# Optimization experiments

Measured on AMD Instinct MI355X. Metric: run time of the kernel, lower is better.

## Reference

```python
import jax, jax.numpy as jnp
import numpy as np

T, H, I, E, K = 1024, 2048, 1024, 16, 2

def setup_inputs() -> dict:
    key = jax.random.key(0)
    ks = jax.random.split(key, 6)
    return {
        "hidden_states": jax.random.normal(ks[0], (T, H), jnp.float32),
        "gate_w": jax.random.normal(ks[1], (E, H), jnp.float32) * 0.02,
        "bias": jax.random.normal(ks[2], (E,), jnp.float32) * 0.01,
        "w1": jax.random.normal(ks[3], (E, H, I), jnp.float32) * 0.02,
        "w3": jax.random.normal(ks[4], (E, H, I), jnp.float32) * 0.02,
        "w2": jax.random.normal(ks[5], (E, I, H), jnp.float32) * 0.02,
    }

def reference(hidden_states, gate_w, bias, w1, w3, w2):
    x = hidden_states  # [T, H]
    # Router gating linear in fp32 (gate.weight cast to float32 in source)
    logits = x.astype(jnp.float32) @ gate_w.T            # [T, E]
    scores = jax.nn.softmax(logits, axis=-1)             # scoring_func='softmax'
    # grouped_topk with num_expert_group=topk_group=1 == plain top-k;
    # e_score_correction_bias only biases expert *selection*.
    _, topk_idx = jax.lax.top_k(scores + bias[None, :], K)   # [T, K]
    topk_w = jnp.take_along_axis(scores, topk_idx, axis=1)   # weights from raw scores
    topk_w = topk_w / jnp.sum(topk_w, axis=-1, keepdims=True)  # renormalize=True
    # Scatter top-k weights into dense combine matrix [T, E]
    rows = jnp.arange(T)[:, None]
    combine = jnp.zeros((T, E), jnp.float32).at[rows, topk_idx].add(topk_w)
    # SwiGLU experts computed densely over all experts, masked by combine
    h1 = jnp.einsum('th,ehi->eti', x, w1)                # [E, T, I]
    h3 = jnp.einsum('th,ehi->eti', x, w3)
    he = jax.nn.silu(h1) * h3
    ye = jnp.einsum('eti,eih->eth', he, w2)              # [E, T, H]
    out = jnp.einsum('eth,te->th', ye, combine.astype(x.dtype))  # weighted combine
    return out
```

## Files before the change

### kernel.cpp

```cpp
#include <hip/hip_runtime.h>
#include <stdint.h>

#define Ttok 1024
#define Hdim 2048
#define Idim 1024
#define Enum 16

typedef __attribute__((ext_vector_type(8))) short  short8;
typedef __attribute__((ext_vector_type(4))) float  f32x4;

#define BAR() asm volatile("s_waitcnt lgkmcnt(0)\n\ts_barrier" ::: "memory")

__device__ __forceinline__ unsigned short f2bf(float f) {
    union { float f; uint32_t u; } v; v.f = f;
    uint32_t u = v.u;
    return (unsigned short)((u + 0x7FFFu + ((u >> 16) & 1u)) >> 16);
}
__device__ __forceinline__ float bf2f(unsigned short h) {
    union { uint32_t u; float f; } v; v.u = ((uint32_t)h) << 16; return v.f;
}
__device__ __forceinline__ uint32_t cvtpk(float lo, float hi) {
    uint32_t d;
    asm("v_cvt_pk_bf16_f32 %0, %1, %2" : "=v"(d) : "v"(lo), "v"(hi));
    return d;
}
__device__ __forceinline__ float silu_mul(unsigned short h1u, unsigned short h3u) {
    float h1 = bf2f(h1u), h3 = bf2f(h3u);
    return h1 * h3 * __builtin_amdgcn_rcpf(1.f + __expf(-h1));
}

__global__ __launch_bounds__(256) void k_router(
    const float* __restrict__ x, const float* __restrict__ gw,
    const float* __restrict__ bias,
    int* __restrict__ counts, int* __restrict__ tids, float* __restrict__ tws)
{
    __shared__ __align__(16) float xrow[Hdim];
    __shared__ float lg[Enum];
    const int t = blockIdx.x;
    const float* xr = x + (size_t)t * Hdim;

    for (int i = threadIdx.x; i < Hdim / 4; i += 256)
        ((f32x4*)xrow)[i] = ((const f32x4*)xr)[i];
    __syncthreads();

    const int lane = threadIdx.x & 63;
    const int wid  = threadIdx.x >> 6;
    for (int e = wid; e < Enum; e += 4) {
        const float* g = gw + (size_t)e * Hdim;
        float s = 0.f;
        for (int j = lane; j < Hdim; j += 64) s += xrow[j] * g[j];
        #pragma unroll
        for (int off = 32; off; off >>= 1) s += __shfl_xor(s, off);
        if (lane == 0) lg[e] = s;
    }
    __syncthreads();

    if (threadIdx.x == 0) {
        float m = lg[0];
        #pragma unroll
        for (int e = 1; e < Enum; ++e) m = fmaxf(m, lg[e]);
        float sc[Enum]; float sum = 0.f;
        #pragma unroll
        for (int e = 0; e < Enum; ++e) { float ex = expf(lg[e] - m); sc[e] = ex; sum += ex; }
        float inv = 1.f / sum;
        #pragma unroll
        for (int e = 0; e < Enum; ++e) sc[e] *= inv;
        int i0 = 0; float b0 = sc[0] + bias[0];
        #pragma unroll
        for (int e = 1; e < Enum; ++e) { float bb = sc[e] + bias[e]; if (bb > b0) { b0 = bb; i0 = e; } }
        int i1 = -1; float b1 = -1e30f;
        #pragma unroll
        for (int e = 0; e < Enum; ++e) {
            if (e == i0) continue;
            float bb = sc[e] + bias[e]; if (bb > b1) { b1 = bb; i1 = e; }
        }
        float w0 = sc[i0], w1v = sc[i1];
        float winv = 1.f / (w0 + w1v);
        w0 *= winv; w1v *= winv;
        int p0 = atomicAdd(&counts[i0], 1);
        tids[i0 * Ttok + p0] = t; tws[i0 * Ttok + p0] = w0;
        int p1 = atomicAdd(&counts[i1], 1);
        tids[i1 * Ttok + p1] = t; tws[i1 * Ttok + p1] = w1v;
    }
}

__global__ __launch_bounds__(256) void k_gather(
    const float* __restrict__ x, const int* __restrict__ counts,
    const int* __restrict__ tids, unsigned short* __restrict__ Xg)
{
    const int p = blockIdx.y;
    int pe = -1, c = 0, acc = 0;
    #pragma unroll
    for (int j = 0; j < Enum; ++j) {
        int nj = (counts[j] + 63) >> 6;
        if (pe < 0 && p < acc + nj) { pe = j; c = p - acc; }
        acc += nj;
    }
    if (pe < 0) return;
    const int Ne = counts[pe];
    const int s  = blockIdx.x;
    const int r  = threadIdx.x & 63;
    const int kq = threadIdx.x >> 6;
    const int row = c * 64 + r;
    const bool valid = row < Ne;
    const int tok = valid ? tids[pe * Ttok + row] : 0;
    const float* xr = x + (size_t)tok * Hdim;

    #pragma unroll
    for (int j = 0; j < 8; ++j) {
        int kg = s * 32 + j * 4 + kq;
        uint4 o = make_uint4(0, 0, 0, 0);
        if (valid) {
            f32x4 p0 = *(const f32x4*)(xr + kg * 8);
            f32x4 p1 = *(const f32x4*)(xr + kg * 8 + 4);
            o.x = cvtpk(p0[0], p0[1]); o.y = cvtpk(p0[2], p0[3]);
            o.z = cvtpk(p1[0], p1[1]); o.w = cvtpk(p1[2], p1[3]);
        }
        *(uint4*)(Xg + ((size_t)(p * 256 + kg) * 64 + r) * 8) = o;
    }
}

union ShH {
    struct {
        unsigned short Xs[2][4096];
        unsigned short Ws[2][8][64][8];
    } a;
    unsigned short T[64][80];
};

__global__ __launch_bounds__(256, 4) void k_h(
    const unsigned short* __restrict__ Xg,
    const float* __restrict__ w1, const float* __restrict__ w3,
    const int* __restrict__ counts,
    unsigned short* __restrict__ H1, unsigned short* __restrict__ H3)
{
    const int e  = blockIdx.z;
    const int Ne = counts[e];
    const int c  = blockIdx.y;
    if (c * 64 >= Ne) return;
    int poff = 0;
    #pragma unroll
    for (int j = 0; j < Enum; ++j) if (j < e) poff += (counts[j] + 63) >> 6;
    const int pc   = poff + c;
    const int mat  = blockIdx.x >> 4;
    const int cb   = blockIdx.x & 15;
    const int col0 = cb * 64;
    const int tid  = threadIdx.x;
    const int lane = tid & 63;
    const int wid  = tid >> 6;
    const int l15  = lane & 15;
    const int kq   = lane >> 4;

    __shared__ ShH sh;

    const unsigned short* xsrc = Xg + (size_t)pc * 131072;
    const int wkg = tid >> 5;
    const int wcp = (tid & 31) * 2;
    const float* wsrc = (mat ? w3 : w1)
        + ((size_t)e * Hdim + wkg * 8) * Idim + col0 + wcp;
    unsigned short* Hm = mat ? H3 : H1;

    f32x4 acc[4];
    #pragma unroll
    for (int a = 0; a < 4; ++a) acc[a] = (f32x4)(0.f);

    const int NK = Hdim / 64;

    auto xload = [&](int ks, short8& v0, short8& v1) {
        const unsigned short* p = xsrc + (size_t)ks * 4096;
        v0 = *(const short8*)(p + tid * 8);
        v1 = *(const short8*)(p + 2048 + tid * 8);
    };
    auto wload = [&](int ks, float2* wv) {
        const float* wp = wsrc + (size_t)ks * 64 * Idim;
        #pragma unroll
        for (int j = 0; j < 8; ++j) wv[j] = *(const float2*)(wp + (size_t)j * Idim);
    };
    auto stage = [&](int buf, short8 x0, short8 x1, const float2* wv) {
        *(short8*)&sh.a.Xs[buf][tid * 8]        = x0;
        *(short8*)&sh.a.Xs[buf][2048 + tid * 8] = x1;
        uint4 q0, q1;
        q0.x = cvtpk(wv[0].x, wv[1].x); q0.y = cvtpk(wv[2].x, wv[3].x);
        q0.z = cvtpk(wv[4].x, wv[5].x); q0.w = cvtpk(wv[6].x, wv[7].x);
        q1.x = cvtpk(wv[0].y, wv[1].y); q1.y = cvtpk(wv[2].y, wv[3].y);
        q1.z = cvtpk(wv[4].y, wv[5].y); q1.w = cvtpk(wv[6].y, wv[7].y);
        *(uint4*)&sh.a.Ws[buf][wkg][wcp][0]     = q0;
        *(uint4*)&sh.a.Ws[buf][wkg][wcp + 1][0] = q1;
    };
    auto mfma_step = [&](int buf) {
        #pragma unroll
        for (int ks2 = 0; ks2 < 2; ++ks2) {
            const int kgi = ks2 * 4 + kq;
            short8 b = *(const short8*)&sh.a.Ws[buf][kgi][wid * 16 + l15][0];
            #pragma unroll
            for (int fr = 0; fr < 4; ++fr) {
                short8 af = *(const short8*)&sh.a.Xs[buf][kgi * 512 + (fr * 16 + l15) * 8];
                acc[fr] = __builtin_amdgcn_mfma_f32_16x16x32_bf16(af, b, acc[fr], 0, 0, 0);
            }
        }
    };

    short8 xA0, xA1, xB0, xB1;
    float2 wA[8], wB[8];
    xload(0, xA0, xA1); wload(0, wA);
    xload(1, xB0, xB1); wload(1, wB);
    stage(0, xA0, xA1, wA);
    BAR();

    for (int ks = 0; ks < NK; ks += 2) {
        if (ks + 2 < NK) { xload(ks + 2, xA0, xA1); wload(ks + 2, wA); }
        mfma_step(0);
        stage(1, xB0, xB1, wB);
        BAR();
        if (ks + 3 < NK) { xload(ks + 3, xB0, xB1); wload(ks + 3, wB); }
        mfma_step(1);
        if (ks + 2 < NK) stage(0, xA0, xA1, wA);
        BAR();
    }

    #pragma unroll
    for (int fr = 0; fr < 4; ++fr)
        #pragma unroll
        for (int k = 0; k < 4; ++k)
            sh.T[fr * 16 + kq * 4 + k][wid * 16 + l15] = f2bf(acc[fr][k]);
    __syncthreads();
    {
        const int r = tid & 63, kgw = tid >> 6;
        #pragma unroll
        for (int q = 0; q < 2; ++q) {
            int KGl = kgw * 2 + q;
            short8 v = *(const short8*)&sh.T[r][KGl * 8];
            *(short8*)(Hm + ((size_t)(pc * 128 + cb * 8 + KGl) * 64 + r) * 8) = v;
        }
    }
}

__global__ __launch_bounds__(256, 4) void k_o(
    const unsigned short* __restrict__ H1, const unsigned short* __restrict__ H3,
    const float* __restrict__ w2,
    const int* __restrict__ counts, const int* __restrict__ tids,
    const float* __restrict__ tws,
    float* __restrict__ out)
{
    const int e  = blockIdx.z;
    const int Ne = counts[e];
    const int c  = blockIdx.y;
    if (c * 64 >= Ne) return;
    int poff = 0;
    #pragma unroll
    for (int j = 0; j < Enum; ++j) if (j < e) poff += (counts[j] + 63) >> 6;
    const int pc   = poff + c;
    const int col0 = blockIdx.x * 64;
    const int tid  = threadIdx.x;
    const int lane = tid & 63;
    const int wid  = tid >> 6;
    const int l15  = lane & 15;
    const int kq   = lane >> 4;

    __shared__ __align__(16) unsigned short As[2][4096];
    __shared__ __align__(16) unsigned short Ws[2][8][64][8];

    const unsigned short* h1src = H1 + (size_t)pc * 65536;
    const unsigned short* h3src = H3 + (size_t)pc * 65536;
    const int wkg = tid >> 5;
    const int wcp = (tid & 31) * 2;
    const float* wsrc = w2 + ((size_t)e * Idim + wkg * 8) * Hdim + col0 + wcp;

    f32x4 acc[4];
    #pragma unroll
    for (int a = 0; a < 4; ++a) acc[a] = (f32x4)(0.f);

    const int NK = Idim / 64;

    auto hload = [&](int ks, short8& a0, short8& a1, short8& b0, short8& b1) {
        a0 = *(const short8*)(h1src + (size_t)ks * 4096 + tid * 8);
        a1 = *(const short8*)(h1src + (size_t)ks * 4096 + 2048 + tid * 8);
        b0 = *(const short8*)(h3src + (size_t)ks * 4096 + tid * 8);
        b1 = *(const short8*)(h3src + (size_t)ks * 4096 + 2048 + tid * 8);
    };
    auto wload = [&](int ks, float2* wv) {
        const float* wp = wsrc + (size_t)ks * 64 * Hdim;
        #pragma unroll
        for (int j = 0; j < 8; ++j) wv[j] = *(const float2*)(wp + (size_t)j * Hdim);
    };
    auto stage = [&](int buf, short8 h10, short8 h11, short8 h30, short8 h31,
                     const float2* wv) {
        uint4 o0, o1;
        o0.x = cvtpk(silu_mul(h10[0], h30[0]), silu_mul(h10[1], h30[1]));
        o0.y = cvtpk(silu_mul(h10[2], h30[2]), silu_mul(h10[3], h30[3]));
        o0.z = cvtpk(silu_mul(h10[4], h30[4]), silu_mul(h10[5], h30[5]));
        o0.w = cvtpk(silu_mul(h10[6], h30[6]), silu_mul(h10[7], h30[7]));
        o1.x = cvtpk(silu_mul(h11[0], h31[0]), silu_mul(h11[1], h31[1]));
        o1.y = cvtpk(silu_mul(h11[2], h31[2]), silu_mul(h11[3], h31[3]));
        o1.z = cvtpk(silu_mul(h11[4], h31[4]), silu_mul(h11[5], h31[5]));
        o1.w = cvtpk(silu_mul(h11[6], h31[6]), silu_mul(h11[7], h31[7]));
        *(uint4*)&As[buf][tid * 8]        = o0;
        *(uint4*)&As[buf][2048 + tid * 8] = o1;
        uint4 q0, q1;
        q0.x = cvtpk(wv[0].x, wv[1].x); q0.y = cvtpk(wv[2].x, wv[3].x);
        q0.z = cvtpk(wv[4].x, wv[5].x); q0.w = cvtpk(wv[6].x, wv[7].x);
        q1.x = cvtpk(wv[0].y, wv[1].y); q1.y = cvtpk(wv[2].y, wv[3].y);
        q1.z = cvtpk(wv[4].y, wv[5].y); q1.w = cvtpk(wv[6].y, wv[7].y);
        *(uint4*)&Ws[buf][wkg][wcp][0]     = q0;
        *(uint4*)&Ws[buf][wkg][wcp + 1][0] = q1;
    };
    auto mfma_step = [&](int buf) {
        #pragma unroll
        for (int ks2 = 0; ks2 < 2; ++ks2) {
            const int kgi = ks2 * 4 + kq;
            short8 b = *(const short8*)&Ws[buf][kgi][wid * 16 + l15][0];
            #pragma unroll
            for (int fr = 0; fr < 4; ++fr) {
                short8 af = *(const short8*)&As[buf][kgi * 512 + (fr * 16 + l15) * 8];
                acc[fr] = __builtin_amdgcn_mfma_f32_16x16x32_bf16(af, b, acc[fr], 0, 0, 0);
            }
        }
    };

    short8 h1A0, h1A1, h3A0, h3A1, h1B0, h1B1, h3B0, h3B1;
    float2 wA[8], wB[8];
    hload(0, h1A0, h1A1, h3A0, h3A1); wload(0, wA);
    hload(1, h1B0, h1B1, h3B0, h3B1); wload(1, wB);
    stage(0, h1A0, h1A1, h3A0, h3A1, wA);
    BAR();

    for (int ks = 0; ks < NK; ks += 2) {
        if (ks + 2 < NK) { hload(ks + 2, h1A0, h1A1, h3A0, h3A1); wload(ks + 2, wA); }
        mfma_step(0);
        stage(1, h1B0, h1B1, h3B0, h3B1, wB);
        BAR();
        if (ks + 3 < NK) { hload(ks + 3, h1B0, h1B1, h3B0, h3B1); wload(ks + 3, wB); }
        mfma_step(1);
        if (ks + 2 < NK) stage(0, h1A0, h1A1, h3A0, h3A1, wA);
        BAR();
    }

    #pragma unroll
    for (int fr = 0; fr < 4; ++fr) {
        #pragma unroll
        for (int k = 0; k < 4; ++k) {
            int grow = c * 64 + fr * 16 + kq * 4 + k;
            if (grow < Ne) {
                int   tk = tids[e * Ttok + grow];
                float w  = tws[e * Ttok + grow];
                atomicAdd(&out[(size_t)tk * Hdim + col0 + wid * 16 + l15], w * acc[fr][k]);
            }
        }
    }
}

extern "C" void kernel_launch(void* const* d_in, const int* in_sizes, int n_in,
                              void* d_out, int out_size, void* d_ws, size_t ws_size,
                              hipStream_t stream)
{
    const float* x    = (const float*)d_in[0];
    const float* gw   = (const float*)d_in[1];
    const float* bias = (const float*)d_in[2];
    const float* w1   = (const float*)d_in[3];
    const float* w3   = (const float*)d_in[4];
    const float* w2   = (const float*)d_in[5];
    float* out = (float*)d_out;

    char* ws = (char*)d_ws;
    int*            counts = (int*)ws;
    int*            tids   = (int*)(ws + 1024);
    float*          tws    = (float*)(ws + 66560);
    unsigned short* Xg     = (unsigned short*)(ws + 132096);
    unsigned short* H1     = (unsigned short*)(ws + 12715008);
    unsigned short* H3     = (unsigned short*)(ws + 19006464);

    hipMemsetAsync(counts, 0, Enum * sizeof(int), stream);
    hipMemsetAsync(out, 0, (size_t)Ttok * Hdim * sizeof(float), stream);

    k_router<<<dim3(Ttok), dim3(256), 0, stream>>>(x, gw, bias, counts, tids, tws);
    k_gather<<<dim3(8, 48), dim3(256), 0, stream>>>(x, counts, tids, Xg);
    k_h<<<dim3(32, 16, Enum), dim3(256), 0, stream>>>(Xg, w1, w3, counts, H1, H3);
    k_o<<<dim3(32, 16, Enum), dim3(256), 0, stream>>>(H1, H3, w2, counts, tids, tws, out);
}
```

Baseline: 254.7 us.

## Deepen weight prefetch to four stages in expert GEMMs and pin scheduling

Both expert GEMM kernels now keep four register buffers of fp32 weight tiles in flight instead of two, so weight loads are issued three k-steps ahead, and the main loop is unrolled by four. Scheduling barriers stop the compiler from moving loads across the MFMA and stage phases. Launch bounds drop from 4 to 2 blocks per SIMD to make room for the extra registers, trading occupancy for deeper memory latency hiding. The x/h loads in the first phase of each iteration are no longer guarded, which assumes the k-step count is a multiple of four.

```diff
diff --git a/kernel.cpp b/kernel.cpp
--- a/kernel.cpp
+++ b/kernel.cpp
@@ -9,7 +9,8 @@
 typedef __attribute__((ext_vector_type(8))) short  short8;
 typedef __attribute__((ext_vector_type(4))) float  f32x4;
 
-#define BAR() asm volatile("s_waitcnt lgkmcnt(0)\n\ts_barrier" ::: "memory")
+#define BAR()  asm volatile("s_waitcnt lgkmcnt(0)\n\ts_barrier" ::: "memory")
+#define SBAR() __builtin_amdgcn_sched_barrier(0)
 
 __device__ __forceinline__ unsigned short f2bf(float f) {
     union { float f; uint32_t u; } v; v.f = f;
@@ -128,7 +129,7 @@
     unsigned short T[64][80];
 };
 
-__global__ __launch_bounds__(256, 4) void k_h(
+__global__ __launch_bounds__(256, 2) void k_h(
     const unsigned short* __restrict__ Xg,
     const float* __restrict__ w1, const float* __restrict__ w3,
     const int* __restrict__ counts,
@@ -200,21 +201,43 @@
         }
     };
 
+    float2 wA[8], wB[8], wC[8], wD[8];
     short8 xA0, xA1, xB0, xB1;
-    float2 wA[8], wB[8];
-    xload(0, xA0, xA1); wload(0, wA);
-    xload(1, xB0, xB1); wload(1, wB);
+
+    wload(0, wA); wload(1, wB); wload(2, wC); wload(3, wD);
+    xload(0, xA0, xA1); xload(1, xB0, xB1);
+    SBAR();
     stage(0, xA0, xA1, wA);
     BAR();
 
-    for (int ks = 0; ks < NK; ks += 2) {
-        if (ks + 2 < NK) { xload(ks + 2, xA0, xA1); wload(ks + 2, wA); }
+    for (int ks = 0; ks < NK; ks += 4) {
+        if (ks + 4 < NK) wload(ks + 4, wA);
+        xload(ks + 2, xA0, xA1);
+        SBAR();
         mfma_step(0);
         stage(1, xB0, xB1, wB);
-        BAR();
-        if (ks + 3 < NK) { xload(ks + 3, xB0, xB1); wload(ks + 3, wB); }
+        SBAR();
+        BAR();
+        if (ks + 5 < NK) wload(ks + 5, wB);
+        if (ks + 3 < NK) xload(ks + 3, xB0, xB1);
+        SBAR();
         mfma_step(1);
-        if (ks + 2 < NK) stage(0, xA0, xA1, wA);
+        stage(0, xA0, xA1, wC);
+        SBAR();
+        BAR();
+        if (ks + 6 < NK) wload(ks + 6, wC);
+        if (ks + 4 < NK) xload(ks + 4, xA0, xA1);
+        SBAR();
+        mfma_step(0);
+        stage(1, xB0, xB1, wD);
+        SBAR();
+        BAR();
+        if (ks + 7 < NK) wload(ks + 7, wD);
+        if (ks + 5 < NK) xload(ks + 5, xB0, xB1);
+        SBAR();
+        mfma_step(1);
+        if (ks + 4 < NK) stage(0, xA0, xA1, wA);
+        SBAR();
         BAR();
     }
 
@@ -235,7 +258,7 @@
     }
 }
 
-__global__ __launch_bounds__(256, 4) void k_o(
+__global__ __launch_bounds__(256, 2) void k_o(
     const unsigned short* __restrict__ H1, const unsigned short* __restrict__ H3,
     const float* __restrict__ w2,
     const int* __restrict__ counts, const int* __restrict__ tids,
@@ -317,21 +340,44 @@
         }
     };
 
+    float2 wA[8], wB[8], wC[8], wD[8];
     short8 h1A0, h1A1, h3A0, h3A1, h1B0, h1B1, h3B0, h3B1;
-    float2 wA[8], wB[8];
-    hload(0, h1A0, h1A1, h3A0, h3A1); wload(0, wA);
-    hload(1, h1B0, h1B1, h3B0, h3B1); wload(1, wB);
+
+    wload(0, wA); wload(1, wB); wload(2, wC); wload(3, wD);
+    hload(0, h1A0, h1A1, h3A0, h3A1);
+    hload(1, h1B0, h1B1, h3B0, h3B1);
+    SBAR();
     stage(0, h1A0, h1A1, h3A0, h3A1, wA);
     BAR();
 
-    for (int ks = 0; ks < NK; ks += 2) {
-        if (ks + 2 < NK) { hload(ks + 2, h1A0, h1A1, h3A0, h3A1); wload(ks + 2, wA); }
+    for (int ks = 0; ks < NK; ks += 4) {
+        if (ks + 4 < NK) wload(ks + 4, wA);
+        hload(ks + 2, h1A0, h1A1, h3A0, h3A1);
+        SBAR();
         mfma_step(0);
         stage(1, h1B0, h1B1, h3B0, h3B1, wB);
-        BAR();
-        if (ks + 3 < NK) { hload(ks + 3, h1B0, h1B1, h3B0, h3B1); wload(ks + 3, wB); }
+        SBAR();
+        BAR();
+        if (ks + 5 < NK) wload(ks + 5, wB);
+        if (ks + 3 < NK) hload(ks + 3, h1B0, h1B1, h3B0, h3B1);
+        SBAR();
         mfma_step(1);
-        if (ks + 2 < NK) stage(0, h1A0, h1A1, h3A0, h3A1, wA);
+        stage(0, h1A0, h1A1, h3A0, h3A1, wC);
+        SBAR();
+        BAR();
+        if (ks + 6 < NK) wload(ks + 6, wC);
+        if (ks + 4 < NK) hload(ks + 4, h1A0, h1A1, h3A0, h3A1);
+        SBAR();
+        mfma_step(0);
+        stage(1, h1B0, h1B1, h3B0, h3B1, wD);
+        SBAR();
+        BAR();
+        if (ks + 7 < NK) wload(ks + 7, wD);
+        if (ks + 5 < NK) hload(ks + 5, h1B0, h1B1, h3B0, h3B1);
+        SBAR();
+        mfma_step(1);
+        if (ks + 4 < NK) stage(0, h1A0, h1A1, h3A0, h3A1, wA);
+        SBAR();
         BAR();
     }
 
```

After: 266.9 us. 4.8% more time.

## Retile expert GEMMs to 192x128 blocks with register-direct A and 4-stage pipeline

Applied to the files above, without the earlier changes.

Both expert GEMM kernels move from 64x64 tiles with 256 threads to 192-row by 128-column tiles with 512 threads. Each fp32 weight tile is now streamed once per 192 tokens instead of once per 64, which cuts redundant weight traffic. In k_h the activation fragments are loaded straight from global memory into registers, skipping the LDS staging. Weight prefetch becomes a 4-deep register rotation with sched_barrier fences. The trade-offs are higher register pressure, lower occupancy, and a grid of only two row blocks per expert, so any expert routed more than 384 tokens would be silently truncated.

```diff
diff --git a/kernel.cpp b/kernel.cpp
--- a/kernel.cpp
+++ b/kernel.cpp
@@ -5,11 +5,14 @@
 #define Hdim 2048
 #define Idim 1024
 #define Enum 16
+#define NKH  64
+#define NKO  32
 
 typedef __attribute__((ext_vector_type(8))) short  short8;
 typedef __attribute__((ext_vector_type(4))) float  f32x4;
 
-#define BAR() asm volatile("s_waitcnt lgkmcnt(0)\n\ts_barrier" ::: "memory")
+#define BAR()  asm volatile("s_waitcnt lgkmcnt(0)\n\ts_barrier" ::: "memory")
+#define SBAR() __builtin_amdgcn_sched_barrier(0)
 
 __device__ __forceinline__ unsigned short f2bf(float f) {
     union { float f; uint32_t u; } v; v.f = f;
@@ -120,15 +123,7 @@
     }
 }
 
-union ShH {
-    struct {
-        unsigned short Xs[2][4096];
-        unsigned short Ws[2][8][64][8];
-    } a;
-    unsigned short T[64][80];
-};
-
-__global__ __launch_bounds__(256, 4) void k_h(
+__global__ __launch_bounds__(512, 2) void k_h(
     const unsigned short* __restrict__ Xg,
     const float* __restrict__ w1, const float* __restrict__ w3,
     const int* __restrict__ counts,
@@ -136,106 +131,125 @@
 {
     const int e  = blockIdx.z;
     const int Ne = counts[e];
-    const int c  = blockIdx.y;
-    if (c * 64 >= Ne) return;
+    const int rb = blockIdx.y;
+    if (rb * 192 >= Ne) return;
     int poff = 0;
     #pragma unroll
     for (int j = 0; j < Enum; ++j) if (j < e) poff += (counts[j] + 63) >> 6;
-    const int pc   = poff + c;
-    const int mat  = blockIdx.x >> 4;
-    const int cb   = blockIdx.x & 15;
-    const int col0 = cb * 64;
+    const int NC   = (Ne + 63) >> 6;
+    const int mat  = blockIdx.x >> 3;
+    const int cb   = blockIdx.x & 7;
+    const int col0 = cb * 128;
     const int tid  = threadIdx.x;
     const int lane = tid & 63;
     const int wid  = tid >> 6;
     const int l15  = lane & 15;
     const int kq   = lane >> 4;
-
-    __shared__ ShH sh;
-
-    const unsigned short* xsrc = Xg + (size_t)pc * 131072;
-    const int wkg = tid >> 5;
-    const int wcp = (tid & 31) * 2;
-    const float* wsrc = (mat ? w3 : w1)
-        + ((size_t)e * Hdim + wkg * 8) * Idim + col0 + wcp;
+    const int wr   = wid >> 2, wc = wid & 3;
+
+    __shared__ __align__(16) unsigned short Ws[2][4096];
+
+    const int cW = tid & 127, gW = tid >> 7;
+    const float* wp = (mat ? w3 : w1) + ((size_t)e * Hdim + gW * 8) * Idim + col0 + cW;
+
+    const unsigned short* aptr[6];
+    int chValid[6];
+    #pragma unroll
+    for (int fr = 0; fr < 6; ++fr) {
+        int row = wr * 96 + fr * 16 + l15;
+        int cgl = rb * 3 + (row >> 6);
+        chValid[fr] = (cgl < NC);
+        int cc = chValid[fr] ? cgl : NC - 1;
+        aptr[fr] = Xg + (((size_t)(poff + cc) * 256 + kq) * 64 + (row & 63)) * 8;
+    }
+
+    f32x4 acc[6][2];
+    #pragma unroll
+    for (int a = 0; a < 6; ++a) { acc[a][0] = (f32x4)(0.f); acc[a][1] = (f32x4)(0.f); }
+
+    float w0r[8], w1r[8], w2r[8], w3r[8];
+    short8 aA[6], aB[6];
+
+    auto WLOAD = [&](int s, float* d) {
+        s = s < NKH ? s : NKH - 1;
+        const float* p = wp + (size_t)s * 32 * Idim;
+        #pragma unroll
+        for (int j = 0; j < 8; ++j) d[j] = p[(size_t)j * Idim];
+    };
+    auto ALOAD = [&](int s, short8* d) {
+        s = s < NKH ? s : NKH - 1;
+        #pragma unroll
+        for (int fr = 0; fr < 6; ++fr) d[fr] = *(const short8*)(aptr[fr] + (size_t)s * 2048);
+    };
+    auto WSTAGE = [&](int buf, const float* w) {
+        uint4 q;
+        q.x = cvtpk(w[0], w[1]); q.y = cvtpk(w[2], w[3]);
+        q.z = cvtpk(w[4], w[5]); q.w = cvtpk(w[6], w[7]);
+        *(uint4*)&Ws[buf][(gW * 128 + cW) * 8] = q;
+    };
+    auto MFMA = [&](int buf, const short8* a) {
+        short8 b0 = *(const short8*)&Ws[buf][(kq * 128 + wc * 32 + l15) * 8];
+        short8 b1 = *(const short8*)&Ws[buf][(kq * 128 + wc * 32 + 16 + l15) * 8];
+        #pragma unroll
+        for (int fr = 0; fr < 6; ++fr) {
+            acc[fr][0] = __builtin_amdgcn_mfma_f32_16x16x32_bf16(a[fr], b0, acc[fr][0], 0, 0, 0);
+            acc[fr][1] = __builtin_amdgcn_mfma_f32_16x16x32_bf16(a[fr], b1, acc[fr][1], 0, 0, 0);
+        }
+    };
+
+    WLOAD(0, w0r); WLOAD(1, w1r); WLOAD(2, w2r);
+    ALOAD(0, aA);
+    SBAR();
+    WSTAGE(0, w0r);
+    BAR();
+
+    for (int ks = 0; ks < NKH; ks += 4) {
+        ALOAD(ks + 1, aB); SBAR();
+        WLOAD(ks + 3, w3r); SBAR();
+        MFMA(0, aA);
+        WSTAGE(1, w1r); SBAR();
+        BAR();
+
+        ALOAD(ks + 2, aA); SBAR();
+        WLOAD(ks + 4, w0r); SBAR();
+        MFMA(1, aB);
+        WSTAGE(0, w2r); SBAR();
+        BAR();
+
+        ALOAD(ks + 3, aB); SBAR();
+        WLOAD(ks + 5, w1r); SBAR();
+        MFMA(0, aA);
+        WSTAGE(1, w3r); SBAR();
+        BAR();
+
+        ALOAD(ks + 4, aA); SBAR();
+        WLOAD(ks + 6, w2r); SBAR();
+        MFMA(1, aB);
+        WSTAGE(0, w0r); SBAR();
+        BAR();
+    }
+
     unsigned short* Hm = mat ? H3 : H1;
-
-    f32x4 acc[4];
-    #pragma unroll
-    for (int a = 0; a < 4; ++a) acc[a] = (f32x4)(0.f);
-
-    const int NK = Hdim / 64;
-
-    auto xload = [&](int ks, short8& v0, short8& v1) {
-        const unsigned short* p = xsrc + (size_t)ks * 4096;
-        v0 = *(const short8*)(p + tid * 8);
-        v1 = *(const short8*)(p + 2048 + tid * 8);
-    };
-    auto wload = [&](int ks, float2* wv) {
-        const float* wp = wsrc + (size_t)ks * 64 * Idim;
-        #pragma unroll
-        for (int j = 0; j < 8; ++j) wv[j] = *(const float2*)(wp + (size_t)j * Idim);
-    };
-    auto stage = [&](int buf, short8 x0, short8 x1, const float2* wv) {
-        *(short8*)&sh.a.Xs[buf][tid * 8]        = x0;
-        *(short8*)&sh.a.Xs[buf][2048 + tid * 8] = x1;
-        uint4 q0, q1;
-        q0.x = cvtpk(wv[0].x, wv[1].x); q0.y = cvtpk(wv[2].x, wv[3].x);
-        q0.z = cvtpk(wv[4].x, wv[5].x); q0.w = cvtpk(wv[6].x, wv[7].x);
-        q1.x = cvtpk(wv[0].y, wv[1].y); q1.y = cvtpk(wv[2].y, wv[3].y);
-        q1.z = cvtpk(wv[4].y, wv[5].y); q1.w = cvtpk(wv[6].y, wv[7].y);
-        *(uint4*)&sh.a.Ws[buf][wkg][wcp][0]     = q0;
-        *(uint4*)&sh.a.Ws[buf][wkg][wcp + 1][0] = q1;
-    };
-    auto mfma_step = [&](int buf) {
-        #pragma unroll
-        for (int ks2 = 0; ks2 < 2; ++ks2) {
-            const int kgi = ks2 * 4 + kq;
-            short8 b = *(const short8*)&sh.a.Ws[buf][kgi][wid * 16 + l15][0];
+    #pragma unroll
+    for (int fr = 0; fr < 6; ++fr) {
+        if (chValid[fr]) {
+            int row = wr * 96 + fr * 16 + l15;
+            int cc  = rb * 3 + (row >> 6);
+            size_t chbase = (size_t)(poff + cc) * 128;
+            int rb0 = ((wr * 96 + fr * 16) & 63) + kq * 4;
             #pragma unroll
-            for (int fr = 0; fr < 4; ++fr) {
-                short8 af = *(const short8*)&sh.a.Xs[buf][kgi * 512 + (fr * 16 + l15) * 8];
-                acc[fr] = __builtin_amdgcn_mfma_f32_16x16x32_bf16(af, b, acc[fr], 0, 0, 0);
+            for (int fc = 0; fc < 2; ++fc) {
+                int colg = col0 + wc * 32 + fc * 16 + l15;
+                size_t kgbase = (chbase + (colg >> 3)) * 512 + (colg & 7);
+                #pragma unroll
+                for (int k = 0; k < 4; ++k)
+                    Hm[kgbase + (size_t)(rb0 + k) * 8] = f2bf(acc[fr][fc][k]);
             }
         }
-    };
-
-    short8 xA0, xA1, xB0, xB1;
-    float2 wA[8], wB[8];
-    xload(0, xA0, xA1); wload(0, wA);
-    xload(1, xB0, xB1); wload(1, wB);
-    stage(0, xA0, xA1, wA);
-    BAR();
-
-    for (int ks = 0; ks < NK; ks += 2) {
-        if (ks + 2 < NK) { xload(ks + 2, xA0, xA1); wload(ks + 2, wA); }
-        mfma_step(0);
-        stage(1, xB0, xB1, wB);
-        BAR();
-        if (ks + 3 < NK) { xload(ks + 3, xB0, xB1); wload(ks + 3, wB); }
-        mfma_step(1);
-        if (ks + 2 < NK) stage(0, xA0, xA1, wA);
-        BAR();
-    }
-
-    #pragma unroll
-    for (int fr = 0; fr < 4; ++fr)
-        #pragma unroll
-        for (int k = 0; k < 4; ++k)
-            sh.T[fr * 16 + kq * 4 + k][wid * 16 + l15] = f2bf(acc[fr][k]);
-    __syncthreads();
-    {
-        const int r = tid & 63, kgw = tid >> 6;
-        #pragma unroll
-        for (int q = 0; q < 2; ++q) {
-            int KGl = kgw * 2 + q;
-            short8 v = *(const short8*)&sh.T[r][KGl * 8];
-            *(short8*)(Hm + ((size_t)(pc * 128 + cb * 8 + KGl) * 64 + r) * 8) = v;
-        }
-    }
-}
-
-__global__ __launch_bounds__(256, 4) void k_o(
+    }
+}
+
+__global__ __launch_bounds__(512, 2) void k_o(
     const unsigned short* __restrict__ H1, const unsigned short* __restrict__ H3,
     const float* __restrict__ w2,
     const int* __restrict__ counts, const int* __restrict__ tids,
@@ -244,106 +258,133 @@
 {
     const int e  = blockIdx.z;
     const int Ne = counts[e];
-    const int c  = blockIdx.y;
-    if (c * 64 >= Ne) return;
+    const int rb = blockIdx.y;
+    if (rb * 192 >= Ne) return;
     int poff = 0;
     #pragma unroll
     for (int j = 0; j < Enum; ++j) if (j < e) poff += (counts[j] + 63) >> 6;
-    const int pc   = poff + c;
-    const int col0 = blockIdx.x * 64;
+    const int NC   = (Ne + 63) >> 6;
+    const int col0 = blockIdx.x * 128;
     const int tid  = threadIdx.x;
     const int lane = tid & 63;
     const int wid  = tid >> 6;
     const int l15  = lane & 15;
     const int kq   = lane >> 4;
-
-    __shared__ __align__(16) unsigned short As[2][4096];
-    __shared__ __align__(16) unsigned short Ws[2][8][64][8];
-
-    const unsigned short* h1src = H1 + (size_t)pc * 65536;
-    const unsigned short* h3src = H3 + (size_t)pc * 65536;
-    const int wkg = tid >> 5;
-    const int wcp = (tid & 31) * 2;
-    const float* wsrc = w2 + ((size_t)e * Idim + wkg * 8) * Hdim + col0 + wcp;
-
-    f32x4 acc[4];
-    #pragma unroll
-    for (int a = 0; a < 4; ++a) acc[a] = (f32x4)(0.f);
-
-    const int NK = Idim / 64;
-
-    auto hload = [&](int ks, short8& a0, short8& a1, short8& b0, short8& b1) {
-        a0 = *(const short8*)(h1src + (size_t)ks * 4096 + tid * 8);
-        a1 = *(const short8*)(h1src + (size_t)ks * 4096 + 2048 + tid * 8);
-        b0 = *(const short8*)(h3src + (size_t)ks * 4096 + tid * 8);
-        b1 = *(const short8*)(h3src + (size_t)ks * 4096 + 2048 + tid * 8);
-    };
-    auto wload = [&](int ks, float2* wv) {
-        const float* wp = wsrc + (size_t)ks * 64 * Hdim;
-        #pragma unroll
-        for (int j = 0; j < 8; ++j) wv[j] = *(const float2*)(wp + (size_t)j * Hdim);
-    };
-    auto stage = [&](int buf, short8 h10, short8 h11, short8 h30, short8 h31,
-                     const float2* wv) {
-        uint4 o0, o1;
-        o0.x = cvtpk(silu_mul(h10[0], h30[0]), silu_mul(h10[1], h30[1]));
-        o0.y = cvtpk(silu_mul(h10[2], h30[2]), silu_mul(h10[3], h30[3]));
-        o0.z = cvtpk(silu_mul(h10[4], h30[4]), silu_mul(h10[5], h30[5]));
-        o0.w = cvtpk(silu_mul(h10[6], h30[6]), silu_mul(h10[7], h30[7]));
-        o1.x = cvtpk(silu_mul(h11[0], h31[0]), silu_mul(h11[1], h31[1]));
-        o1.y = cvtpk(silu_mul(h11[2], h31[2]), silu_mul(h11[3], h31[3]));
-        o1.z = cvtpk(silu_mul(h11[4], h31[4]), silu_mul(h11[5], h31[5]));
-        o1.w = cvtpk(silu_mul(h11[6], h31[6]), silu_mul(h11[7], h31[7]));
-        *(uint4*)&As[buf][tid * 8]        = o0;
-        *(uint4*)&As[buf][2048 + tid * 8] = o1;
-        uint4 q0, q1;
-        q0.x = cvtpk(wv[0].x, wv[1].x); q0.y = cvtpk(wv[2].x, wv[3].x);
-        q0.z = cvtpk(wv[4].x, wv[5].x); q0.w = cvtpk(wv[6].x, wv[7].x);
-        q1.x = cvtpk(wv[0].y, wv[1].y); q1.y = cvtpk(wv[2].y, wv[3].y);
-        q1.z = cvtpk(wv[4].y, wv[5].y); q1.w = cvtpk(wv[6].y, wv[7].y);
-        *(uint4*)&Ws[buf][wkg][wcp][0]     = q0;
-        *(uint4*)&Ws[buf][wkg][wcp + 1][0] = q1;
-    };
-    auto mfma_step = [&](int buf) {
-        #pragma unroll
-        for (int ks2 = 0; ks2 < 2; ++ks2) {
-            const int kgi = ks2 * 4 + kq;
-            short8 b = *(const short8*)&Ws[buf][kgi][wid * 16 + l15][0];
-            #pragma unroll
-            for (int fr = 0; fr < 4; ++fr) {
-                short8 af = *(const short8*)&As[buf][kgi * 512 + (fr * 16 + l15) * 8];
-                acc[fr] = __builtin_amdgcn_mfma_f32_16x16x32_bf16(af, b, acc[fr], 0, 0, 0);
+    const int wr   = wid >> 2, wc = wid & 3;
+
+    __shared__ __align__(16) unsigned short Ws[2][4096];
+    __shared__ __align__(16) unsigned short As[2][6144];
+
+    const int cW = tid & 127, gW = tid >> 7;
+    const float* wp = w2 + ((size_t)e * Idim + gW * 8) * Hdim + col0 + cW;
+
+    const unsigned short* hp1[2]; const unsigned short* hp3[2];
+    int slotOff[2]; bool slotOn[2];
+    #pragma unroll
+    for (int q = 0; q < 2; ++q) {
+        int slot = (q == 0) ? tid : (tid < 256 ? tid + 512 : tid);
+        slotOn[q]  = (q == 0) || (tid < 256);
+        int gs  = slot / 192;
+        int row = slot - gs * 192;
+        int cgl = rb * 3 + (row >> 6);
+        int cc  = cgl < NC ? cgl : NC - 1;
+        size_t base = (((size_t)(poff + cc) * 128 + gs) * 64 + (row & 63)) * 8;
+        hp1[q] = H1 + base; hp3[q] = H3 + base;
+        slotOff[q] = slot * 8;
+    }
+
+    f32x4 acc[6][2];
+    #pragma unroll
+    for (int a = 0; a < 6; ++a) { acc[a][0] = (f32x4)(0.f); acc[a][1] = (f32x4)(0.f); }
+
+    float w0r[8], w1r[8], w2r[8], w3r[8];
+    short8 hA[4], hB[4];
+
+    auto WLOAD = [&](int s, float* d) {
+        s = s < NKO ? s : NKO - 1;
+        const float* p = wp + (size_t)s * 32 * Hdim;
+        #pragma unroll
+        for (int j = 0; j < 8; ++j) d[j] = p[(size_t)j * Hdim];
+    };
+    auto HLOAD = [&](int s, short8* d) {
+        s = s < NKO ? s : NKO - 1;
+        d[0] = *(const short8*)(hp1[0] + (size_t)s * 2048);
+        d[1] = *(const short8*)(hp3[0] + (size_t)s * 2048);
+        d[2] = *(const short8*)(hp1[1] + (size_t)s * 2048);
+        d[3] = *(const short8*)(hp3[1] + (size_t)s * 2048);
+    };
+    auto STAGE = [&](int buf, const short8* h, const float* w) {
+        #pragma unroll
+        for (int q = 0; q < 2; ++q) {
+            if (slotOn[q]) {
+                uint4 o;
+                o.x = cvtpk(silu_mul(h[q*2][0], h[q*2+1][0]), silu_mul(h[q*2][1], h[q*2+1][1]));
+                o.y = cvtpk(silu_mul(h[q*2][2], h[q*2+1][2]), silu_mul(h[q*2][3], h[q*2+1][3]));
+                o.z = cvtpk(silu_mul(h[q*2][4], h[q*2+1][4]), silu_mul(h[q*2][5], h[q*2+1][5]));
+                o.w = cvtpk(silu_mul(h[q*2][6], h[q*2+1][6]), silu_mul(h[q*2][7], h[q*2+1][7]));
+                *(uint4*)&As[buf][slotOff[q]] = o;
             }
         }
-    };
-
-    short8 h1A0, h1A1, h3A0, h3A1, h1B0, h1B1, h3B0, h3B1;
-    float2 wA[8], wB[8];
-    hload(0, h1A0, h1A1, h3A0, h3A1); wload(0, wA);
-    hload(1, h1B0, h1B1, h3B0, h3B1); wload(1, wB);
-    stage(0, h1A0, h1A1, h3A0, h3A1, wA);
+        uint4 qw;
+        qw.x = cvtpk(w[0], w[1]); qw.y = cvtpk(w[2], w[3]);
+        qw.z = cvtpk(w[4], w[5]); qw.w = cvtpk(w[6], w[7]);
+        *(uint4*)&Ws[buf][(gW * 128 + cW) * 8] = qw;
+    };
+    auto MFMA = [&](int buf) {
+        short8 b0 = *(const short8*)&Ws[buf][(kq * 128 + wc * 32 + l15) * 8];
+        short8 b1 = *(const short8*)&Ws[buf][(kq * 128 + wc * 32 + 16 + l15) * 8];
+        #pragma unroll
+        for (int fr = 0; fr < 6; ++fr) {
+            short8 af = *(const short8*)&As[buf][(kq * 192 + wr * 96 + fr * 16 + l15) * 8];
+            acc[fr][0] = __builtin_amdgcn_mfma_f32_16x16x32_bf16(af, b0, acc[fr][0], 0, 0, 0);
+            acc[fr][1] = __builtin_amdgcn_mfma_f32_16x16x32_bf16(af, b1, acc[fr][1], 0, 0, 0);
+        }
+    };
+
+    WLOAD(0, w0r); WLOAD(1, w1r); WLOAD(2, w2r);
+    HLOAD(0, hA); HLOAD(1, hB);
+    SBAR();
+    STAGE(0, hA, w0r);
     BAR();
 
-    for (int ks = 0; ks < NK; ks += 2) {
-        if (ks + 2 < NK) { hload(ks + 2, h1A0, h1A1, h3A0, h3A1); wload(ks + 2, wA); }
-        mfma_step(0);
-        stage(1, h1B0, h1B1, h3B0, h3B1, wB);
-        BAR();
-        if (ks + 3 < NK) { hload(ks + 3, h1B0, h1B1, h3B0, h3B1); wload(ks + 3, wB); }
-        mfma_step(1);
-        if (ks + 2 < NK) stage(0, h1A0, h1A1, h3A0, h3A1, wA);
-        BAR();
-    }
-
-    #pragma unroll
-    for (int fr = 0; fr < 4; ++fr) {
+    for (int ks = 0; ks < NKO; ks += 4) {
+        HLOAD(ks + 2, hA); SBAR();
+        WLOAD(ks + 3, w3r); SBAR();
+        MFMA(0);
+        STAGE(1, hB, w1r); SBAR();
+        BAR();
+
+        HLOAD(ks + 3, hB); SBAR();
+        WLOAD(ks + 4, w0r); SBAR();
+        MFMA(1);
+        STAGE(0, hA, w2r); SBAR();
+        BAR();
+
+        HLOAD(ks + 4, hA); SBAR();
+        WLOAD(ks + 5, w1r); SBAR();
+        MFMA(0);
+        STAGE(1, hB, w3r); SBAR();
+        BAR();
+
+        HLOAD(ks + 5, hB); SBAR();
+        WLOAD(ks + 6, w2r); SBAR();
+        MFMA(1);
+        STAGE(0, hA, w0r); SBAR();
+        BAR();
+    }
+
+    #pragma unroll
+    for (int fr = 0; fr < 6; ++fr) {
         #pragma unroll
         for (int k = 0; k < 4; ++k) {
-            int grow = c * 64 + fr * 16 + kq * 4 + k;
+            int grow = rb * 192 + wr * 96 + fr * 16 + kq * 4 + k;
             if (grow < Ne) {
                 int   tk = tids[e * Ttok + grow];
                 float w  = tws[e * Ttok + grow];
-                atomicAdd(&out[(size_t)tk * Hdim + col0 + wid * 16 + l15], w * acc[fr][k]);
+                #pragma unroll
+                for (int fc = 0; fc < 2; ++fc)
+                    atomicAdd(&out[(size_t)tk * Hdim + col0 + wc * 32 + fc * 16 + l15],
+                              w * acc[fr][fc][k]);
             }
         }
     }
@@ -374,6 +415,6 @@
 
     k_router<<<dim3(Ttok), dim3(256), 0, stream>>>(x, gw, bias, counts, tids, tws);
     k_gather<<<dim3(8, 48), dim3(256), 0, stream>>>(x, counts, tids, Xg);
-    k_h<<<dim3(32, 16, Enum), dim3(256), 0, stream>>>(Xg, w1, w3, counts, H1, H3);
-    k_o<<<dim3(32, 16, Enum), dim3(256), 0, stream>>>(H1, H3, w2, counts, tids, tws, out);
-}
+    k_h<<<dim3(16, 2, Enum), dim3(512), 0, stream>>>(Xg, w1, w3, counts, H1, H3);
+    k_o<<<dim3(16, 2, Enum), dim3(512), 0, stream>>>(H1, H3, w2, counts, tids, tws, out);
+}
```

Measured after the change: 290.9 us. +14.2%, slower.
